# Optimization experiments

Hardware: AMD Instinct MI355X
Metric: run time of the kernel (lower is better)

The kernel has to match this reference:

```python
import jax, jax.numpy as jnp
import numpy as np

N_NODES = 100000
N_EDGES = 3200000
N_GRAPHS = 128
IN_DIM, HID, OUT = 128, 64, 128


def gcn_conv(x, W, b, src, dst, n_nodes):
    """PyG GCNConv: add self-loops, symmetric deg^-1/2 normalization, scatter-add."""
    xw = x @ W  # [N, H]
    ones = jnp.ones(src.shape[0], dtype=x.dtype)
    deg = jax.ops.segment_sum(ones, dst, num_segments=n_nodes) + 1.0  # +1 self loop
    dinv = jax.lax.rsqrt(deg)
    norm = dinv[src] * dinv[dst]  # [E]
    agg = jax.ops.segment_sum(xw[src] * norm[:, None], dst, num_segments=n_nodes)
    # self-loop contribution: norm = dinv * dinv = 1/deg
    return agg + xw * (1.0 / deg)[:, None] + b


def global_mean_pool(x, batch, n_graphs):
    sums = jax.ops.segment_sum(x, batch, num_segments=n_graphs)
    cnts = jax.ops.segment_sum(jnp.ones(x.shape[0], dtype=x.dtype), batch, num_segments=n_graphs)
    return sums / jnp.maximum(cnts, 1.0)[:, None]


def setup_inputs() -> dict:
    key = jax.random.key(0)
    ks = jax.random.split(key, 9)
    x = jax.random.normal(ks[0], (N_NODES, IN_DIM), dtype=jnp.float32)
    edge_index = jax.random.randint(ks[1], (2, N_EDGES), 0, N_NODES, dtype=jnp.int64)
    batch = jnp.sort(jax.random.randint(ks[2], (N_NODES,), 0, N_GRAPHS, dtype=jnp.int64))
    def glorot(k, shp):
        lim = float(np.sqrt(6.0 / (shp[0] + shp[1])))
        return jax.random.uniform(k, shp, dtype=jnp.float32, minval=-lim, maxval=lim)
    return {
        "x": x,
        "edge_index": edge_index,
        "batch": batch,
        "W1": glorot(ks[3], (IN_DIM, HID)),
        "b1": jnp.zeros((HID,), jnp.float32),
        "W2": glorot(ks[4], (HID, HID)),
        "b2": jnp.zeros((HID,), jnp.float32),
        "Wl": glorot(ks[5], (HID, OUT)),
        "bl": jnp.zeros((OUT,), jnp.float32),
    }


def reference(x, edge_index, batch, W1, b1, W2, b2, Wl, bl):
    src, dst = edge_index[0], edge_index[1]
    h = jax.nn.relu(gcn_conv(x, W1, b1, src, dst, N_NODES))
    h = jax.nn.relu(gcn_conv(h, W2, b2, src, dst, N_NODES))
    g = global_mean_pool(h, batch, N_GRAPHS)  # [G, HID]
    return g @ Wl + bl  # [G, OUT]
```

## Files before the change

kernel.cpp:

```cpp
#include <hip/hip_runtime.h>
#include <math.h>

#define N_NODES    100000
#define N_EDGES    3200000
#define N_GRAPHS   128
#define IN_DIM     128
#define HID        64
#define OUT_DIM    128
#define NSUP       98
#define SUP_SHIFT  10
#define SUP_MASK   1023
#define BIN_BLOCKS 512
#define E_PER_BIN  6250

typedef unsigned short ushort_t;

__device__ __forceinline__ ushort_t f2bf(float f) {
    unsigned int u = __float_as_uint(f);
    u += 0x7FFFu + ((u >> 16) & 1u);
    return (ushort_t)(u >> 16);
}

__global__ __launch_bounds__(256) void k_hist(const int* __restrict__ dst,
                                              int* __restrict__ sup_cnt,
                                              int* __restrict__ hist_mat) {
    __shared__ int hist[NSUP];
    int t = threadIdx.x;
    if (t < NSUP) hist[t] = 0;
    __syncthreads();
    int e0 = blockIdx.x * E_PER_BIN;
    for (int e = e0 + t; e < e0 + E_PER_BIN; e += 256)
        atomicAdd(&hist[dst[e] >> SUP_SHIFT], 1);
    __syncthreads();
    if (t < NSUP) {
        int h = hist[t];
        hist_mat[blockIdx.x * NSUP + t] = h;
        if (h) atomicAdd(&sup_cnt[t], h);
    }
}

__global__ void k_scan_sup(const int* __restrict__ sup_cnt,
                           int* __restrict__ sup_ptr, int* __restrict__ sup_cur) {
    __shared__ int s[128];
    int t = threadIdx.x;
    int v = (t < NSUP) ? sup_cnt[t] : 0;
    s[t] = v; __syncthreads();
    for (int d = 1; d < 128; d <<= 1) {
        int add = (t >= d) ? s[t - d] : 0;
        __syncthreads();
        s[t] += add;
        __syncthreads();
    }
    int excl = s[t] - v;
    if (t <= NSUP) sup_ptr[t] = excl;
    if (t < NSUP)  sup_cur[t] = excl;
}

__global__ __launch_bounds__(256) void k_super(const int* __restrict__ src,
                                               const int* __restrict__ dst,
                                               const int* __restrict__ hist_mat,
                                               int* __restrict__ sup_cursor,
                                               unsigned int* __restrict__ recs) {
    __shared__ int base[NSUP];
    __shared__ int hist[NSUP];
    int t = threadIdx.x;
    int e0 = blockIdx.x * E_PER_BIN;
    if (t < NSUP) {
        int h = hist_mat[blockIdx.x * NSUP + t];
        base[t] = h ? atomicAdd(&sup_cursor[t], h) : 0;
        hist[t] = 0;
    }
    __syncthreads();
    for (int e = e0 + t; e < e0 + E_PER_BIN; e += 256) {
        int d = dst[e];
        int b = d >> SUP_SHIFT;
        int pos = base[b] + atomicAdd(&hist[b], 1);
        recs[pos] = ((unsigned int)src[e] << SUP_SHIFT) | (unsigned int)(d & SUP_MASK);
    }
}

__global__ __launch_bounds__(1024) void k_csrB(const unsigned int* __restrict__ recs,
                                               const int* __restrict__ sup_ptr,
                                               int* __restrict__ row_ptr,
                                               float* __restrict__ dinv,
                                               int* __restrict__ csr_src) {
    __shared__ int lcnt[1024];
    __shared__ int s[1024];
    __shared__ int lcur[1024];
    int b = blockIdx.x, t = threadIdx.x;
    int start = sup_ptr[b], end = sup_ptr[b + 1];
    lcnt[t] = 0;
    __syncthreads();
    for (int i = start + t; i < end; i += 1024)
        atomicAdd(&lcnt[recs[i] & SUP_MASK], 1);
    __syncthreads();
    int v = lcnt[t];
    s[t] = v; __syncthreads();
    for (int d = 1; d < 1024; d <<= 1) {
        int add = (t >= d) ? s[t - d] : 0;
        __syncthreads();
        s[t] += add;
        __syncthreads();
    }
    int excl = s[t] - v;
    int n = b * 1024 + t;
    if (n <= N_NODES) row_ptr[n] = start + excl;
    if (n < N_NODES)  dinv[n] = 1.0f / sqrtf((float)v + 1.0f);
    lcur[t] = start + excl;
    __syncthreads();
    for (int i = start + t; i < end; i += 1024) {
        unsigned int r = recs[i];
        int p = atomicAdd(&lcur[r & SUP_MASK], 1);
        csr_src[p] = (int)(r >> SUP_SHIFT);
    }
}

template <int K>
__global__ __launch_bounds__(256) void k_gemm(const float* __restrict__ X,
                                              const float* __restrict__ W,
                                              const float* __restrict__ dinv,
                                              ushort_t* __restrict__ Ybf, int nrows) {
    __shared__ float Xs[64][65];
    __shared__ float Ws[64][64];
    int t = threadIdx.x;
    int row0 = blockIdx.x * 64;
    int tc = t & 15, tr = t >> 4;
    int c0 = tc * 4, r0 = tr * 4;
    float acc[4][4] = {};
    for (int kc = 0; kc < K; kc += 64) {
        __syncthreads();
#pragma unroll
        for (int i = 0; i < 16; ++i) {
            int e = i * 256 + t;
            int r = e >> 6, k = e & 63;
            int gr = row0 + r;
            Xs[r][k] = (gr < nrows) ? X[(size_t)gr * K + kc + k] : 0.0f;
        }
#pragma unroll
        for (int i = 0; i < 16; ++i) {
            int e = i * 256 + t;
            int k = e >> 6, c = e & 63;
            Ws[k][c] = W[(size_t)(kc + k) * 64 + c];
        }
        __syncthreads();
#pragma unroll 8
        for (int k = 0; k < 64; ++k) {
            float xv[4];
#pragma unroll
            for (int i = 0; i < 4; ++i) xv[i] = Xs[r0 + i][k];
            const float4 w4 = *(const float4*)&Ws[k][c0];
#pragma unroll
            for (int i = 0; i < 4; ++i) {
                acc[i][0] += xv[i] * w4.x;
                acc[i][1] += xv[i] * w4.y;
                acc[i][2] += xv[i] * w4.z;
                acc[i][3] += xv[i] * w4.w;
            }
        }
    }
#pragma unroll
    for (int i = 0; i < 4; ++i) {
        int gr = row0 + r0 + i;
        if (gr < nrows) {
            float dn = dinv[gr];
            ushort4 o;
            o.x = f2bf(dn * acc[i][0]);
            o.y = f2bf(dn * acc[i][1]);
            o.z = f2bf(dn * acc[i][2]);
            o.w = f2bf(dn * acc[i][3]);
            *(ushort4*)(Ybf + (size_t)gr * 64 + c0) = o;
        }
    }
}

__global__ __launch_bounds__(256) void k_gather(const ushort_t* __restrict__ xwp,
                                                const float* __restrict__ dinv,
                                                const int* __restrict__ row_ptr,
                                                const int* __restrict__ csr_src,
                                                const float* __restrict__ bias,
                                                float* __restrict__ hout) {
    int wave = threadIdx.x >> 6;
    int lane = threadIdx.x & 63;
    int n = blockIdx.x * 4 + wave;
    if (n >= N_NODES) return;
    int sub = lane >> 3, c8 = (lane & 7) * 8;
    int start = row_ptr[n], end = row_ptr[n + 1];
    double a[8] = {0.0, 0.0, 0.0, 0.0, 0.0, 0.0, 0.0, 0.0};
    int i = start + sub;
    for (; i + 8 < end; i += 16) {
        int s0 = csr_src[i];
        int s1 = csr_src[i + 8];
        const uint4 v0 = *(const uint4*)(xwp + (size_t)s0 * 64 + c8);
        const uint4 v1 = *(const uint4*)(xwp + (size_t)s1 * 64 + c8);
        a[0] += (double)__uint_as_float(v0.x << 16);
        a[1] += (double)__uint_as_float(v0.x & 0xFFFF0000u);
        a[2] += (double)__uint_as_float(v0.y << 16);
        a[3] += (double)__uint_as_float(v0.y & 0xFFFF0000u);
        a[4] += (double)__uint_as_float(v0.z << 16);
        a[5] += (double)__uint_as_float(v0.z & 0xFFFF0000u);
        a[6] += (double)__uint_as_float(v0.w << 16);
        a[7] += (double)__uint_as_float(v0.w & 0xFFFF0000u);
        a[0] += (double)__uint_as_float(v1.x << 16);
        a[1] += (double)__uint_as_float(v1.x & 0xFFFF0000u);
        a[2] += (double)__uint_as_float(v1.y << 16);
        a[3] += (double)__uint_as_float(v1.y & 0xFFFF0000u);
        a[4] += (double)__uint_as_float(v1.z << 16);
        a[5] += (double)__uint_as_float(v1.z & 0xFFFF0000u);
        a[6] += (double)__uint_as_float(v1.w << 16);
        a[7] += (double)__uint_as_float(v1.w & 0xFFFF0000u);
    }
    if (i < end) {
        int s0 = csr_src[i];
        const uint4 v = *(const uint4*)(xwp + (size_t)s0 * 64 + c8);
        a[0] += (double)__uint_as_float(v.x << 16);
        a[1] += (double)__uint_as_float(v.x & 0xFFFF0000u);
        a[2] += (double)__uint_as_float(v.y << 16);
        a[3] += (double)__uint_as_float(v.y & 0xFFFF0000u);
        a[4] += (double)__uint_as_float(v.z << 16);
        a[5] += (double)__uint_as_float(v.z & 0xFFFF0000u);
        a[6] += (double)__uint_as_float(v.w << 16);
        a[7] += (double)__uint_as_float(v.w & 0xFFFF0000u);
    }
#pragma unroll
    for (int off = 8; off < 64; off <<= 1) {
#pragma unroll
        for (int j = 0; j < 8; ++j) a[j] += __shfl_xor(a[j], off, 64);
    }
    if (sub == 0) {
        float dn = dinv[n];
        const uint4 xn = *(const uint4*)(xwp + (size_t)n * 64 + c8);
        float xnf[8];
        xnf[0] = __uint_as_float(xn.x << 16); xnf[1] = __uint_as_float(xn.x & 0xFFFF0000u);
        xnf[2] = __uint_as_float(xn.y << 16); xnf[3] = __uint_as_float(xn.y & 0xFFFF0000u);
        xnf[4] = __uint_as_float(xn.z << 16); xnf[5] = __uint_as_float(xn.z & 0xFFFF0000u);
        xnf[6] = __uint_as_float(xn.w << 16); xnf[7] = __uint_as_float(xn.w & 0xFFFF0000u);
        float4 b0 = *(const float4*)(bias + c8);
        float4 b1 = *(const float4*)(bias + c8 + 4);
        float4 r0, r1;
        r0.x = fmaxf(dn * ((float)a[0] + xnf[0]) + b0.x, 0.f);
        r0.y = fmaxf(dn * ((float)a[1] + xnf[1]) + b0.y, 0.f);
        r0.z = fmaxf(dn * ((float)a[2] + xnf[2]) + b0.z, 0.f);
        r0.w = fmaxf(dn * ((float)a[3] + xnf[3]) + b0.w, 0.f);
        r1.x = fmaxf(dn * ((float)a[4] + xnf[4]) + b1.x, 0.f);
        r1.y = fmaxf(dn * ((float)a[5] + xnf[5]) + b1.y, 0.f);
        r1.z = fmaxf(dn * ((float)a[6] + xnf[6]) + b1.z, 0.f);
        r1.w = fmaxf(dn * ((float)a[7] + xnf[7]) + b1.w, 0.f);
        *(float4*)(hout + (size_t)n * 64 + c8)     = r0;
        *(float4*)(hout + (size_t)n * 64 + c8 + 4) = r1;
    }
}

__device__ __forceinline__ int lower_bound(const int* __restrict__ a, int n, int key) {
    int lo = 0, hi = n;
    while (lo < hi) {
        int mid = (lo + hi) >> 1;
        if (a[mid] < key) lo = mid + 1; else hi = mid;
    }
    return lo;
}

__global__ __launch_bounds__(1024) void k_pool(const float* __restrict__ h,
                                               const int* __restrict__ batch,
                                               float* __restrict__ g) {
    int b = blockIdx.x;
    int t = threadIdx.x, c = t & 63, rg = t >> 6;
    __shared__ float s[16][64];
    int start = lower_bound(batch, N_NODES, b);
    int end   = lower_bound(batch, N_NODES, b + 1);
    float sum = 0.f;
    for (int n = start + rg; n < end; n += 16) sum += h[(size_t)n * 64 + c];
    s[rg][c] = sum;
    __syncthreads();
    if (rg == 0) {
        float tot = 0.f;
#pragma unroll
        for (int k = 0; k < 16; ++k) tot += s[k][c];
        float cntf = (float)(end - start);
        g[b * 64 + c] = tot / fmaxf(cntf, 1.0f);
    }
}

__global__ void k_final(const float* __restrict__ g, const float* __restrict__ Wl,
                        const float* __restrict__ bl, float* __restrict__ out) {
    __shared__ float gs[64];
    int row = blockIdx.x, c = threadIdx.x;
    if (c < 64) gs[c] = g[row * 64 + c];
    __syncthreads();
    float acc = bl[c];
#pragma unroll
    for (int k = 0; k < 64; ++k) acc += gs[k] * Wl[k * 128 + c];
    out[row * 128 + c] = acc;
}

extern "C" void kernel_launch(void* const* d_in, const int* in_sizes, int n_in,
                              void* d_out, int out_size, void* d_ws, size_t ws_size,
                              hipStream_t stream) {
    const float* x    = (const float*)d_in[0];
    const int*   ei   = (const int*)d_in[1];
    const int*   batch= (const int*)d_in[2];
    const float* W1   = (const float*)d_in[3];
    const float* b1   = (const float*)d_in[4];
    const float* W2   = (const float*)d_in[5];
    const float* b2   = (const float*)d_in[6];
    const float* Wl   = (const float*)d_in[7];
    const float* bl   = (const float*)d_in[8];
    float* out = (float*)d_out;

    const int* src = ei;
    const int* dst = ei + N_EDGES;

    char* base = (char*)d_ws;
    float*        dinv     = (float*)(base + 0);
    int*          row_ptr  = (int*)  (base + 400128);
    int*          sup_cnt  = (int*)  (base + 800256);
    int*          sup_ptr  = (int*)  (base + 802304);
    int*          sup_cur  = (int*)  (base + 804352);
    int*          hist_mat = (int*)  (base + 806400);
    int*          csr_src  = (int*)  (base + 1007616);
    ushort_t*     xwp      = (ushort_t*)(base + 13807616);
    float*        h        = (float*)(base + 26607616);
    float*        g        = (float*)(base + 52207616);
    unsigned int* recs     = (unsigned int*)xwp;

    hipMemsetAsync(sup_cnt, 0, NSUP * sizeof(int), stream);
    k_hist    <<<BIN_BLOCKS, 256, 0, stream>>>(dst, sup_cnt, hist_mat);
    k_scan_sup<<<1, 128, 0, stream>>>(sup_cnt, sup_ptr, sup_cur);
    k_super   <<<BIN_BLOCKS, 256, 0, stream>>>(src, dst, hist_mat, sup_cur, recs);
    k_csrB    <<<NSUP, 1024, 0, stream>>>(recs, sup_ptr, row_ptr, dinv, csr_src);

    const int GEMM_GRID = (N_NODES + 63) / 64;

    k_gemm<IN_DIM><<<GEMM_GRID, 256, 0, stream>>>(x, W1, dinv, xwp, N_NODES);
    k_gather<<<(N_NODES + 3) / 4, 256, 0, stream>>>(xwp, dinv, row_ptr, csr_src, b1, h);

    k_gemm<HID><<<GEMM_GRID, 256, 0, stream>>>(h, W2, dinv, xwp, N_NODES);
    k_gather<<<(N_NODES + 3) / 4, 256, 0, stream>>>(xwp, dinv, row_ptr, csr_src, b2, h);

    k_pool <<<N_GRAPHS, 1024, 0, stream>>>(h, batch, g);
    k_final<<<N_GRAPHS, 128, 0, stream>>>(g, Wl, bl, out);
}
```

Before: 316.6 us.

## Fuse pool with final linear, drop memset, unroll gather by four

Removes the memset and the global atomic supernode count by having the single-block scan kernel reduce the per-block histogram matrix itself. Fuses mean pooling with the final linear layer into one kernel, saving a launch and a global round trip. Adds a 4-way unrolled edge loop in the gather to keep more independent row loads in flight. In exchange, the scan kernel now serially reads 50K histogram entries in one block, and the wider unroll raises register pressure in the gather.

```diff
diff --git a/kernel.cpp b/kernel.cpp
--- a/kernel.cpp
+++ b/kernel.cpp
@@ -22,7 +22,6 @@
 }
 
 __global__ __launch_bounds__(256) void k_hist(const int* __restrict__ dst,
-                                              int* __restrict__ sup_cnt,
                                               int* __restrict__ hist_mat) {
     __shared__ int hist[NSUP];
     int t = threadIdx.x;
@@ -32,28 +31,36 @@
     for (int e = e0 + t; e < e0 + E_PER_BIN; e += 256)
         atomicAdd(&hist[dst[e] >> SUP_SHIFT], 1);
     __syncthreads();
-    if (t < NSUP) {
-        int h = hist[t];
-        hist_mat[blockIdx.x * NSUP + t] = h;
-        if (h) atomicAdd(&sup_cnt[t], h);
-    }
-}
-
-__global__ void k_scan_sup(const int* __restrict__ sup_cnt,
-                           int* __restrict__ sup_ptr, int* __restrict__ sup_cur) {
+    if (t < NSUP) hist_mat[blockIdx.x * NSUP + t] = hist[t];
+}
+
+__global__ __launch_bounds__(512) void k_scan_sup(const int* __restrict__ hist_mat,
+                                                  int* __restrict__ sup_ptr,
+                                                  int* __restrict__ sup_cur) {
+    __shared__ int lsum[NSUP];
     __shared__ int s[128];
     int t = threadIdx.x;
-    int v = (t < NSUP) ? sup_cnt[t] : 0;
-    s[t] = v; __syncthreads();
+    if (t < NSUP) lsum[t] = 0;
+    __syncthreads();
+    for (int i = t; i < BIN_BLOCKS * NSUP; i += 512) {
+        int v = hist_mat[i];
+        if (v) atomicAdd(&lsum[i % NSUP], v);
+    }
+    __syncthreads();
+    if (t < 128) s[t] = (t < NSUP) ? lsum[t] : 0;
+    __syncthreads();
     for (int d = 1; d < 128; d <<= 1) {
-        int add = (t >= d) ? s[t - d] : 0;
-        __syncthreads();
-        s[t] += add;
-        __syncthreads();
-    }
-    int excl = s[t] - v;
-    if (t <= NSUP) sup_ptr[t] = excl;
-    if (t < NSUP)  sup_cur[t] = excl;
+        int add = (t < 128 && t >= d) ? s[t - d] : 0;
+        __syncthreads();
+        if (t < 128) s[t] += add;
+        __syncthreads();
+    }
+    if (t < 128) {
+        int v = (t < NSUP) ? lsum[t] : 0;
+        int excl = s[t] - v;
+        if (t <= NSUP) sup_ptr[t] = excl;
+        if (t < NSUP)  sup_cur[t] = excl;
+    }
 }
 
 __global__ __launch_bounds__(256) void k_super(const int* __restrict__ src,
@@ -172,6 +179,16 @@
         }
     }
 }
+
+#define ACC8(vv)                                        \
+    a[0] += (double)__uint_as_float((vv).x << 16);      \
+    a[1] += (double)__uint_as_float((vv).x & 0xFFFF0000u); \
+    a[2] += (double)__uint_as_float((vv).y << 16);      \
+    a[3] += (double)__uint_as_float((vv).y & 0xFFFF0000u); \
+    a[4] += (double)__uint_as_float((vv).z << 16);      \
+    a[5] += (double)__uint_as_float((vv).z & 0xFFFF0000u); \
+    a[6] += (double)__uint_as_float((vv).w << 16);      \
+    a[7] += (double)__uint_as_float((vv).w & 0xFFFF0000u);
 
 __global__ __launch_bounds__(256) void k_gather(const ushort_t* __restrict__ xwp,
                                                 const float* __restrict__ dinv,
@@ -187,39 +204,28 @@
     int start = row_ptr[n], end = row_ptr[n + 1];
     double a[8] = {0.0, 0.0, 0.0, 0.0, 0.0, 0.0, 0.0, 0.0};
     int i = start + sub;
+    for (; i + 24 < end; i += 32) {
+        int s0 = csr_src[i];
+        int s1 = csr_src[i + 8];
+        int s2 = csr_src[i + 16];
+        int s3 = csr_src[i + 24];
+        const uint4 v0 = *(const uint4*)(xwp + (size_t)s0 * 64 + c8);
+        const uint4 v1 = *(const uint4*)(xwp + (size_t)s1 * 64 + c8);
+        const uint4 v2 = *(const uint4*)(xwp + (size_t)s2 * 64 + c8);
+        const uint4 v3 = *(const uint4*)(xwp + (size_t)s3 * 64 + c8);
+        ACC8(v0) ACC8(v1) ACC8(v2) ACC8(v3)
+    }
     for (; i + 8 < end; i += 16) {
         int s0 = csr_src[i];
         int s1 = csr_src[i + 8];
         const uint4 v0 = *(const uint4*)(xwp + (size_t)s0 * 64 + c8);
         const uint4 v1 = *(const uint4*)(xwp + (size_t)s1 * 64 + c8);
-        a[0] += (double)__uint_as_float(v0.x << 16);
-        a[1] += (double)__uint_as_float(v0.x & 0xFFFF0000u);
-        a[2] += (double)__uint_as_float(v0.y << 16);
-        a[3] += (double)__uint_as_float(v0.y & 0xFFFF0000u);
-        a[4] += (double)__uint_as_float(v0.z << 16);
-        a[5] += (double)__uint_as_float(v0.z & 0xFFFF0000u);
-        a[6] += (double)__uint_as_float(v0.w << 16);
-        a[7] += (double)__uint_as_float(v0.w & 0xFFFF0000u);
-        a[0] += (double)__uint_as_float(v1.x << 16);
-        a[1] += (double)__uint_as_float(v1.x & 0xFFFF0000u);
-        a[2] += (double)__uint_as_float(v1.y << 16);
-        a[3] += (double)__uint_as_float(v1.y & 0xFFFF0000u);
-        a[4] += (double)__uint_as_float(v1.z << 16);
-        a[5] += (double)__uint_as_float(v1.z & 0xFFFF0000u);
-        a[6] += (double)__uint_as_float(v1.w << 16);
-        a[7] += (double)__uint_as_float(v1.w & 0xFFFF0000u);
+        ACC8(v0) ACC8(v1)
     }
     if (i < end) {
         int s0 = csr_src[i];
         const uint4 v = *(const uint4*)(xwp + (size_t)s0 * 64 + c8);
-        a[0] += (double)__uint_as_float(v.x << 16);
-        a[1] += (double)__uint_as_float(v.x & 0xFFFF0000u);
-        a[2] += (double)__uint_as_float(v.y << 16);
-        a[3] += (double)__uint_as_float(v.y & 0xFFFF0000u);
-        a[4] += (double)__uint_as_float(v.z << 16);
-        a[5] += (double)__uint_as_float(v.z & 0xFFFF0000u);
-        a[6] += (double)__uint_as_float(v.w << 16);
-        a[7] += (double)__uint_as_float(v.w & 0xFFFF0000u);
+        ACC8(v)
     }
 #pragma unroll
     for (int off = 8; off < 64; off <<= 1) {
@@ -259,12 +265,15 @@
     return lo;
 }
 
-__global__ __launch_bounds__(1024) void k_pool(const float* __restrict__ h,
-                                               const int* __restrict__ batch,
-                                               float* __restrict__ g) {
+__global__ __launch_bounds__(1024) void k_poolfinal(const float* __restrict__ h,
+                                                    const int* __restrict__ batch,
+                                                    const float* __restrict__ Wl,
+                                                    const float* __restrict__ bl,
+                                                    float* __restrict__ out) {
     int b = blockIdx.x;
     int t = threadIdx.x, c = t & 63, rg = t >> 6;
     __shared__ float s[16][64];
+    __shared__ float gs[64];
     int start = lower_bound(batch, N_NODES, b);
     int end   = lower_bound(batch, N_NODES, b + 1);
     float sum = 0.f;
@@ -275,21 +284,15 @@
         float tot = 0.f;
 #pragma unroll
         for (int k = 0; k < 16; ++k) tot += s[k][c];
-        float cntf = (float)(end - start);
-        g[b * 64 + c] = tot / fmaxf(cntf, 1.0f);
-    }
-}
-
-__global__ void k_final(const float* __restrict__ g, const float* __restrict__ Wl,
-                        const float* __restrict__ bl, float* __restrict__ out) {
-    __shared__ float gs[64];
-    int row = blockIdx.x, c = threadIdx.x;
-    if (c < 64) gs[c] = g[row * 64 + c];
-    __syncthreads();
-    float acc = bl[c];
-#pragma unroll
-    for (int k = 0; k < 64; ++k) acc += gs[k] * Wl[k * 128 + c];
-    out[row * 128 + c] = acc;
+        gs[c] = tot / fmaxf((float)(end - start), 1.0f);
+    }
+    __syncthreads();
+    if (t < 128) {
+        float acc = bl[t];
+#pragma unroll
+        for (int k = 0; k < 64; ++k) acc += gs[k] * Wl[k * 128 + t];
+        out[b * 128 + t] = acc;
+    }
 }
 
 extern "C" void kernel_launch(void* const* d_in, const int* in_sizes, int n_in,
@@ -312,19 +315,16 @@
     char* base = (char*)d_ws;
     float*        dinv     = (float*)(base + 0);
     int*          row_ptr  = (int*)  (base + 400128);
-    int*          sup_cnt  = (int*)  (base + 800256);
-    int*          sup_ptr  = (int*)  (base + 802304);
-    int*          sup_cur  = (int*)  (base + 804352);
-    int*          hist_mat = (int*)  (base + 806400);
-    int*          csr_src  = (int*)  (base + 1007616);
-    ushort_t*     xwp      = (ushort_t*)(base + 13807616);
-    float*        h        = (float*)(base + 26607616);
-    float*        g        = (float*)(base + 52207616);
+    int*          sup_ptr  = (int*)  (base + 800256);
+    int*          sup_cur  = (int*)  (base + 802304);
+    int*          hist_mat = (int*)  (base + 804352);
+    int*          csr_src  = (int*)  (base + 1005568);
+    ushort_t*     xwp      = (ushort_t*)(base + 13805568);
+    float*        h        = (float*)(base + 26605568);
     unsigned int* recs     = (unsigned int*)xwp;
 
-    hipMemsetAsync(sup_cnt, 0, NSUP * sizeof(int), stream);
-    k_hist    <<<BIN_BLOCKS, 256, 0, stream>>>(dst, sup_cnt, hist_mat);
-    k_scan_sup<<<1, 128, 0, stream>>>(sup_cnt, sup_ptr, sup_cur);
+    k_hist    <<<BIN_BLOCKS, 256, 0, stream>>>(dst, hist_mat);
+    k_scan_sup<<<1, 512, 0, stream>>>(hist_mat, sup_ptr, sup_cur);
     k_super   <<<BIN_BLOCKS, 256, 0, stream>>>(src, dst, hist_mat, sup_cur, recs);
     k_csrB    <<<NSUP, 1024, 0, stream>>>(recs, sup_ptr, row_ptr, dinv, csr_src);
 
@@ -336,6 +336,5 @@
     k_gemm<HID><<<GEMM_GRID, 256, 0, stream>>>(h, W2, dinv, xwp, N_NODES);
     k_gather<<<(N_NODES + 3) / 4, 256, 0, stream>>>(xwp, dinv, row_ptr, csr_src, b2, h);
 
-    k_pool <<<N_GRAPHS, 1024, 0, stream>>>(h, batch, g);
-    k_final<<<N_GRAPHS, 128, 0, stream>>>(g, Wl, bl, out);
-}
+    k_poolfinal<<<N_GRAPHS, 1024, 0, stream>>>(h, batch, Wl, bl, out);
+}
```

Measured after the change: 340.1 us. +7.4%, slower.
